# Kernel optimization log

Measured on AMD Instinct MI355X. Metric: run time of the kernel, lower is better.

Reference implementation:

```python
import jax, jax.numpy as jnp
import numpy as np

NUM_CLASSES = 1000
TEMPERATURE = 0.1
B, B_OOD, D = 4096, 4096, 512


def _l2norm(x):
    return x / jnp.linalg.norm(x, axis=-1, keepdims=True)


def setup_inputs() -> dict:
    key = jax.random.key(0)
    k1, k2, k3, k4, k5 = jax.random.split(key, 5)
    return {
        "centers1": _l2norm(jax.random.normal(k1, (NUM_CLASSES, D), dtype=jnp.float32)),
        "features": _l2norm(jax.random.normal(k2, (B, D), dtype=jnp.float32)),
        "targets": jax.random.randint(k3, (B,), 0, NUM_CLASSES, dtype=jnp.int64 if jax.config.jax_enable_x64 else jnp.int32),
        "features_ood": _l2norm(jax.random.normal(k4, (B_OOD, D), dtype=jnp.float32)),
        "pseudo_target_ood": jax.random.randint(k5, (B_OOD,), 0, NUM_CLASSES, dtype=jnp.int64 if jax.config.jax_enable_x64 else jnp.int32),
    }


def reference(centers1, features, targets, features_ood, pseudo_target_ood):
    C = centers1.shape[0]
    b = features.shape[0]
    bo = features_ood.shape[0]
    n = b + C + bo  # total anchors: batch + class centers + ood

    centers_lbl = jnp.arange(C, dtype=targets.dtype)
    ood_lbl = jnp.full((bo,), C, dtype=targets.dtype)  # ood gets label == num_classes
    targets_all = jnp.concatenate([targets, centers_lbl, ood_lbl])              # [N]
    targets_all_class = jnp.concatenate([targets, centers_lbl, pseudo_target_ood])  # [N]

    # per-class count over all N labels (pseudo labels for ood)
    batch_cls_count = jnp.zeros((C,), dtype=jnp.float32).at[targets_all_class].add(1.0)

    # positive mask: same label as anchor, excluding self (diagonal for j < B)
    mask = (targets_all[:b, None] == targets_all[None, :]).astype(jnp.float32)  # [B,N]
    logits_mask = 1.0 - (jnp.arange(n)[None, :] == jnp.arange(b)[:, None]).astype(jnp.float32)
    mask = mask * logits_mask

    features_all = jnp.concatenate([features, centers1, features_ood], axis=0)  # [N,D]
    logits = jnp.matmul(features, features_all.T) / TEMPERATURE                 # [B,N]
    logits = logits - jax.lax.stop_gradient(jnp.max(logits, axis=1, keepdims=True))

    exp_logits = jnp.exp(logits) * logits_mask
    # class-balanced per-instance weight (count of the column's class, minus positive mask)
    per_ins_weight = batch_cls_count[targets_all_class][None, :] - mask         # [B,N]
    exp_logits_sum = jnp.sum(exp_logits / per_ins_weight, axis=1, keepdims=True)
    log_prob = logits - jnp.log(exp_logits_sum)

    mean_log_prob_pos = jnp.sum(mask * log_prob, axis=1) / jnp.sum(mask, axis=1)
    loss = -jnp.mean(mean_log_prob_pos)
    return loss
```

## Files before the change

kernel.cpp:

```cpp
#include <hip/hip_runtime.h>
#include <stdint.h>

#define NUM_C 1000
#define NB    4096
#define NCOL  9192
#define NPAD  9216
#define DK    512
#define BM    128
#define BN    256
#define INV_T 10.0f

typedef __attribute__((ext_vector_type(4))) float f32x4;

#define OFF_FALL  0u
#define OFF_CNT   4718592u
#define OFF_CNTT  4722688u
#define OFF_S     4726784u
#define OFF_P     4743168u

__device__ __forceinline__ void async16(const void* g, void* l) {
  __builtin_amdgcn_global_load_lds((const __attribute__((address_space(1))) void*)g,
                                   (__attribute__((address_space(3))) void*)l,
                                   16, 0, 0);
}

__device__ __forceinline__ unsigned sw_e4m3(float x) {
  float ax = fabsf(x);
  unsigned s = (__float_as_uint(x) >> 24) & 0x80u;
  if (ax < 0.015625f) {
    int n = (int)rintf(ax * 512.0f);
    if (n >= 8) return s | 0x08u;
    return s | (unsigned)n;
  }
  if (ax >= 448.0f) return s | 0x7Eu;
  unsigned u = __float_as_uint(ax);
  int ee = (int)(u >> 23) - 127;
  float scale = __uint_as_float((unsigned)(3 - ee + 127) << 23);
  int qv = (int)rintf(ax * scale);
  if (qv == 16) { ee++; qv = 8; }
  return s | (unsigned)(((ee + 7) << 3) | (qv - 8));
}

template <bool HI>
__device__ __forceinline__ int cvt2(float a, float b, int old) {
#if __has_builtin(__builtin_amdgcn_cvt_pk_fp8_f32)
  return __builtin_amdgcn_cvt_pk_fp8_f32(a, b, old, HI);
#else
  unsigned pk = sw_e4m3(a) | (sw_e4m3(b) << 8);
  return HI ? (int)(((unsigned)old & 0x0000FFFFu) | (pk << 16))
            : (int)(((unsigned)old & 0xFFFF0000u) | pk);
#endif
}

__device__ __forceinline__ long long mk_ll(unsigned lo, unsigned hi) {
  return (long long)(((unsigned long long)hi << 32) | lo);
}

__global__ __launch_bounds__(256) void prep_k(const float* __restrict__ centers,
                                              const float* __restrict__ feats,
                                              const float* __restrict__ ood,
                                              const int* __restrict__ targets,
                                              const int* __restrict__ pseudo,
                                              uint4* __restrict__ fall,
                                              unsigned* __restrict__ cnt,
                                              unsigned* __restrict__ cntT,
                                              float* __restrict__ SP) {
  __shared__ unsigned hc[1024];
  __shared__ unsigned hct[1024];
  const int tid = threadIdx.x;

  int idx  = blockIdx.x * 256 + tid;
  int lane = idx & 63;
  int kp   = (idx >> 6) & 7;
  int t    = idx >> 9;
  int row  = t * 16 + (lane & 15);
  int k0   = kp * 64 + (lane >> 4) * 8;

  const float* src = nullptr;
  if (row < NB)              src = feats   + (size_t)row * DK;
  else if (row < NB + NUM_C) src = centers + (size_t)(row - NB) * DK;
  else if (row < NCOL)       src = ood     + (size_t)(row - NB - NUM_C) * DK;
  uint4 out = make_uint4(0u, 0u, 0u, 0u);
  if (src) {
    float4 v0 = *(const float4*)(src + k0);
    float4 v1 = *(const float4*)(src + k0 + 4);
    float4 v2 = *(const float4*)(src + k0 + 32);
    float4 v3 = *(const float4*)(src + k0 + 36);
    int p;
    p = 0; p = cvt2<false>(v0.x, v0.y, p); p = cvt2<true>(v0.z, v0.w, p); out.x = (unsigned)p;
    p = 0; p = cvt2<false>(v1.x, v1.y, p); p = cvt2<true>(v1.z, v1.w, p); out.y = (unsigned)p;
    p = 0; p = cvt2<false>(v2.x, v2.y, p); p = cvt2<true>(v2.z, v2.w, p); out.z = (unsigned)p;
    p = 0; p = cvt2<false>(v3.x, v3.y, p); p = cvt2<true>(v3.z, v3.w, p); out.w = (unsigned)p;
  }
  fall[idx] = out;

  if (blockIdx.x < 16) {
    for (int kk = tid; kk < 1024; kk += 256) { hc[kk] = 0u; hct[kk] = 0u; }
    __syncthreads();
    int i = blockIdx.x * 256 + tid;
    int tt = targets[i];
    atomicAdd(&hc[tt], 1u);
    atomicAdd(&hct[tt], 1u);
    atomicAdd(&hc[pseudo[i]], 1u);
    __syncthreads();
    for (int kk = tid; kk < 1024; kk += 256) {
      unsigned c = hc[kk], ct = hct[kk];
      if (c)  atomicAdd(&cnt[kk], c);
      if (ct) atomicAdd(&cntT[kk], ct);
    }
  } else if (blockIdx.x < 48) {
    SP[(blockIdx.x - 16) * 256 + tid] = 0.0f;
  }
}

__global__ __launch_bounds__(256, 2) void gemm_fused(const unsigned char* __restrict__ fall,
                                                     const int* __restrict__ targets,
                                                     const int* __restrict__ pseudo,
                                                     const unsigned* __restrict__ cnt,
                                                     float* __restrict__ Sacc,
                                                     float* __restrict__ Pacc) {
  __shared__ unsigned char Alds[65536];
  __shared__ int    sLbl[BN];
  __shared__ float  sRw0[BN];
  __shared__ float  sRw1[BN];
  __shared__ int    sTgt[BM];

  const int tid   = threadIdx.x;
  const int nTile = blockIdx.x;
  const int mTile = blockIdx.y;
  const int lane  = tid & 63;
  const int wv    = tid >> 6;
  const int wm    = wv >> 1;
  const int wn    = wv & 1;
  const int q     = lane >> 4;
  const int cIdx  = lane & 15;

  {
    const unsigned char* aSrc = fall + (size_t)(mTile * 8) * 8192;
#pragma unroll
    for (int i = 0; i < 16; i++)
      async16(aSrc + (i * 256 + tid) * 16, &Alds[(i * 256 + tid) * 16]);
  }

  {
    int j = nTile * BN + tid;
    int lbl, tac;
    if (j >= NCOL)         { lbl = -1; tac = -1; }
    else if (j < NB)       { tac = targets[j]; lbl = tac; }
    else if (j < NB+NUM_C) { tac = j - NB;     lbl = tac; }
    else                   { tac = pseudo[j - NB - NUM_C]; lbl = NUM_C; }
    sLbl[tid] = lbl;
    if (tac >= 0) {
      float w = (float)(1u + cnt[tac]);
      sRw0[tid] = 1.0f / w;
      sRw1[tid] = 1.0f / (w - 1.0f);
    } else {
      sRw0[tid] = 0.f;
      sRw1[tid] = 0.f;
    }
    if (tid < BM) sTgt[tid] = targets[mTile * BM + tid];
  }

  f32x4 acc[4][8];
#pragma unroll
  for (int mi = 0; mi < 4; mi++)
#pragma unroll
    for (int ni = 0; ni < 8; ni++)
      acc[mi][ni] = (f32x4){0.f, 0.f, 0.f, 0.f};

  const unsigned char* bBase = fall + (size_t)(nTile * 16 + wn * 8) * 8192 + lane * 16;
  const unsigned aBase = (unsigned)(wm * 4) * 8192u + (unsigned)lane * 16u;

  uint4 bCur[8], bNxt[8];
#pragma unroll
  for (int ni = 0; ni < 8; ni++)
    bCur[ni] = *(const uint4*)(bBase + ni * 8192);

  __syncthreads();

#pragma unroll
  for (int kp = 0; kp < 8; kp++) {
    if (kp < 7) {
#pragma unroll
      for (int ni = 0; ni < 8; ni++)
        bNxt[ni] = *(const uint4*)(bBase + ni * 8192 + (kp + 1) * 1024);
    }
    long long af0[4], af1[4];
#pragma unroll
    for (int mi = 0; mi < 4; mi++) {
      af0[mi] = *(const long long*)&Alds[aBase + mi * 8192 + kp * 1024];
      af1[mi] = *(const long long*)&Alds[aBase + mi * 8192 + kp * 1024 + 8];
    }
#pragma unroll
    for (int mi = 0; mi < 4; mi++)
#pragma unroll
      for (int ni = 0; ni < 8; ni++)
        acc[mi][ni] = __builtin_amdgcn_mfma_f32_16x16x32_fp8_fp8(af0[mi], mk_ll(bCur[ni].x, bCur[ni].y), acc[mi][ni], 0, 0, 0);
#pragma unroll
    for (int mi = 0; mi < 4; mi++)
#pragma unroll
      for (int ni = 0; ni < 8; ni++)
        acc[mi][ni] = __builtin_amdgcn_mfma_f32_16x16x32_fp8_fp8(af1[mi], mk_ll(bCur[ni].z, bCur[ni].w), acc[mi][ni], 0, 0, 0);
    if (kp < 7) {
#pragma unroll
      for (int ni = 0; ni < 8; ni++) bCur[ni] = bNxt[ni];
    }
  }

  float vS[16], vP[16];
#pragma unroll
  for (int s = 0; s < 16; s++) { vS[s] = 0.f; vP[s] = 0.f; }

#pragma unroll
  for (int ni = 0; ni < 8; ni++) {
    int jloc = wn * 128 + ni * 16 + cIdx;
    int j    = nTile * BN + jloc;
    int lblj = sLbl[jloc];
    float rw0 = sRw0[jloc], rw1 = sRw1[jloc];
#pragma unroll
    for (int mi = 0; mi < 4; mi++) {
      f32x4 a = acc[mi][ni];
#pragma unroll
      for (int r = 0; r < 4; r++) {
        int iloc = wm * 64 + mi * 16 + q * 4 + r;
        int i    = mTile * BM + iloc;
        int ti   = sTgt[iloc];
        float l  = a[r] * INV_T;
        bool diag = (j == i);
        bool pos  = (lblj == ti) && !diag;
        float rw  = diag ? 0.0f : (pos ? rw1 : rw0);
        float e   = __expf(l - 10.0f) * rw;
        vS[mi * 4 + r] += e;
        vP[mi * 4 + r] += pos ? l : 0.0f;
      }
    }
  }

#define RED_STEP(m, s, h)                                        \
  {                                                              \
    float sendS = (cIdx & (m)) ? vS[(s)] : vS[(s) + (h)];        \
    float sendP = (cIdx & (m)) ? vP[(s)] : vP[(s) + (h)];        \
    float rS = __shfl_xor(sendS, (m), 64);                       \
    float rP = __shfl_xor(sendP, (m), 64);                       \
    vS[(s)] = ((cIdx & (m)) ? vS[(s) + (h)] : vS[(s)]) + rS;     \
    vP[(s)] = ((cIdx & (m)) ? vP[(s) + (h)] : vP[(s)]) + rP;     \
  }
  RED_STEP(8, 0, 8) RED_STEP(8, 1, 8) RED_STEP(8, 2, 8) RED_STEP(8, 3, 8)
  RED_STEP(8, 4, 8) RED_STEP(8, 5, 8) RED_STEP(8, 6, 8) RED_STEP(8, 7, 8)
  RED_STEP(4, 0, 4) RED_STEP(4, 1, 4) RED_STEP(4, 2, 4) RED_STEP(4, 3, 4)
  RED_STEP(2, 0, 2) RED_STEP(2, 1, 2)
  RED_STEP(1, 0, 1)
#undef RED_STEP

  {
    int rowLoc = wm * 64 + (cIdx >> 2) * 16 + q * 4 + (cIdx & 3);
    int i = mTile * BM + rowLoc;
    atomicAdd(&Sacc[i], vS[0]);
    atomicAdd(&Pacc[i], vP[0]);
  }
}

__global__ __launch_bounds__(256) void finalize_k(const float* __restrict__ S,
                                                  const float* __restrict__ P,
                                                  const int* __restrict__ targets,
                                                  const unsigned* __restrict__ cntT,
                                                  float* __restrict__ out) {
  __shared__ unsigned ct[1024];
  __shared__ float red[4];
  int tid = threadIdx.x;
  for (int k = tid; k < 1024; k += 256) ct[k] = cntT[k];
  __syncthreads();
  float local = 0.f;
  for (int i = tid; i < NB; i += 256) {
    float npos = (float)ct[targets[i]];
    local += P[i] / npos - INV_T - __logf(S[i]);
  }
  for (int m = 1; m < 64; m <<= 1) local += __shfl_xor(local, m, 64);
  if ((tid & 63) == 0) red[tid >> 6] = local;
  __syncthreads();
  if (tid == 0) {
    float t = red[0] + red[1] + red[2] + red[3];
    out[0] = -t / (float)NB;
  }
}

extern "C" void kernel_launch(void* const* d_in, const int* in_sizes, int n_in,
                              void* d_out, int out_size, void* d_ws, size_t ws_size,
                              hipStream_t stream) {
  const float* centers = (const float*)d_in[0];
  const float* feats   = (const float*)d_in[1];
  const int*   targets = (const int*)d_in[2];
  const float* ood     = (const float*)d_in[3];
  const int*   pseudo  = (const int*)d_in[4];

  char* ws = (char*)d_ws;
  uint4*    fall  = (uint4*)(ws + OFF_FALL);
  unsigned* cnt   = (unsigned*)(ws + OFF_CNT);
  unsigned* cntT  = (unsigned*)(ws + OFF_CNTT);
  float*    Sacc  = (float*)(ws + OFF_S);
  float*    Pacc  = (float*)(ws + OFF_P);

  hipMemsetAsync(ws + OFF_CNT, 0, 8192, stream);
  prep_k<<<dim3((NPAD * 32) / 256), 256, 0, stream>>>(centers, feats, ood, targets, pseudo,
                                                      fall, cnt, cntT, Sacc);
  gemm_fused<<<dim3(NPAD / BN, NB / BM), 256, 0, stream>>>((const unsigned char*)fall, targets,
                                                           pseudo, cnt, Sacc, Pacc);
  finalize_k<<<1, 256, 0, stream>>>(Sacc, Pacc, targets, cntT, (float*)d_out);
}
```

Baseline: 120.9 us.

## Switch GEMM to 32x32x64 scaled FP8 MFMA with swizzled operand layout

Replaces the 16x16x32 FP8 MFMA with the MI355 32x32x64 f8f6f4 scaled MFMA using neutral scales. The prep kernel now writes operands in a new XOR-swizzled 32-row packed layout that matches this instruction, so LDS reads avoid bank conflicts. Workgroup indices are also remapped for better L2 reuse. The epilogue and row reduction are rewritten around the new 32x32 accumulator layout. The aim is fewer, denser matrix instructions and less LDS traffic, at the cost of a more intricate index mapping that must stay correct.

Measured after the change: 119.5 us. No clear change (-1.1%).

```diff
diff --git a/kernel.cpp b/kernel.cpp
--- a/kernel.cpp
+++ b/kernel.cpp
@@ -10,7 +10,8 @@
 #define BN    256
 #define INV_T 10.0f
 
-typedef __attribute__((ext_vector_type(4))) float f32x4;
+typedef __attribute__((ext_vector_type(16))) float f32x16;
+typedef __attribute__((ext_vector_type(8)))  int   i32x8;
 
 #define OFF_FALL  0u
 #define OFF_CNT   4718592u
@@ -52,9 +53,15 @@
 #endif
 }
 
-__device__ __forceinline__ long long mk_ll(unsigned lo, unsigned hi) {
-  return (long long)(((unsigned long long)hi << 32) | lo);
-}
+__device__ __forceinline__ i32x8 mk8(uint4 lo, uint4 hi) {
+  i32x8 r;
+  r[0] = (int)lo.x; r[1] = (int)lo.y; r[2] = (int)lo.z; r[3] = (int)lo.w;
+  r[4] = (int)hi.x; r[5] = (int)hi.y; r[6] = (int)hi.z; r[7] = (int)hi.w;
+  return r;
+}
+
+#define MFMA_SC(a, b, c) \
+  __builtin_amdgcn_mfma_scale_f32_32x32x64_f8f6f4((a), (b), (c), 0, 0, 0, 0x7F7F7F7F, 0, 0x7F7F7F7F)
 
 __global__ __launch_bounds__(256) void prep_k(const float* __restrict__ centers,
                                               const float* __restrict__ feats,
@@ -70,11 +77,13 @@
   const int tid = threadIdx.x;
 
   int idx  = blockIdx.x * 256 + tid;
-  int lane = idx & 63;
-  int kp   = (idx >> 6) & 7;
-  int t    = idx >> 9;
-  int row  = t * 16 + (lane & 15);
-  int k0   = kp * 64 + (lane >> 4) * 8;
+  int tile = idx >> 10;
+  int kq   = (idx >> 7) & 7;
+  int p    = idx & 127;
+  int c    = p ^ ((p >> 3) & 7);
+  int lane = c >> 1;
+  int row  = tile * 32 + (lane & 31);
+  int k0   = kq * 64 + (lane >> 5) * 32 + (c & 1) * 16;
 
   const float* src = nullptr;
   if (row < NB)              src = feats   + (size_t)row * DK;
@@ -84,13 +93,13 @@
   if (src) {
     float4 v0 = *(const float4*)(src + k0);
     float4 v1 = *(const float4*)(src + k0 + 4);
-    float4 v2 = *(const float4*)(src + k0 + 32);
-    float4 v3 = *(const float4*)(src + k0 + 36);
-    int p;
-    p = 0; p = cvt2<false>(v0.x, v0.y, p); p = cvt2<true>(v0.z, v0.w, p); out.x = (unsigned)p;
-    p = 0; p = cvt2<false>(v1.x, v1.y, p); p = cvt2<true>(v1.z, v1.w, p); out.y = (unsigned)p;
-    p = 0; p = cvt2<false>(v2.x, v2.y, p); p = cvt2<true>(v2.z, v2.w, p); out.z = (unsigned)p;
-    p = 0; p = cvt2<false>(v3.x, v3.y, p); p = cvt2<true>(v3.z, v3.w, p); out.w = (unsigned)p;
+    float4 v2 = *(const float4*)(src + k0 + 8);
+    float4 v3 = *(const float4*)(src + k0 + 12);
+    int q;
+    q = 0; q = cvt2<false>(v0.x, v0.y, q); q = cvt2<true>(v0.z, v0.w, q); out.x = (unsigned)q;
+    q = 0; q = cvt2<false>(v1.x, v1.y, q); q = cvt2<true>(v1.z, v1.w, q); out.y = (unsigned)q;
+    q = 0; q = cvt2<false>(v2.x, v2.y, q); q = cvt2<true>(v2.z, v2.w, q); out.z = (unsigned)q;
+    q = 0; q = cvt2<false>(v3.x, v3.y, q); q = cvt2<true>(v3.z, v3.w, q); out.w = (unsigned)q;
   }
   fall[idx] = out;
 
@@ -104,8 +113,8 @@
     atomicAdd(&hc[pseudo[i]], 1u);
     __syncthreads();
     for (int kk = tid; kk < 1024; kk += 256) {
-      unsigned c = hc[kk], ct = hct[kk];
-      if (c)  atomicAdd(&cnt[kk], c);
+      unsigned cc = hc[kk], ct = hct[kk];
+      if (cc) atomicAdd(&cnt[kk], cc);
       if (ct) atomicAdd(&cntT[kk], ct);
     }
   } else if (blockIdx.x < 48) {
@@ -125,18 +134,16 @@
   __shared__ float  sRw1[BN];
   __shared__ int    sTgt[BM];
 
-  const int tid   = threadIdx.x;
-  const int nTile = blockIdx.x;
-  const int mTile = blockIdx.y;
+  const int tid  = threadIdx.x;
+  int flat = (int)blockIdx.y * 36 + (int)blockIdx.x;
+  int swz  = (flat & 7) * 144 + (flat >> 3);
+  const int nTile = swz >> 5;
+  const int mTile = swz & 31;
   const int lane  = tid & 63;
   const int wv    = tid >> 6;
-  const int wm    = wv >> 1;
-  const int wn    = wv & 1;
-  const int q     = lane >> 4;
-  const int cIdx  = lane & 15;
 
   {
-    const unsigned char* aSrc = fall + (size_t)(mTile * 8) * 8192;
+    const unsigned char* aSrc = fall + (size_t)mTile * 65536;
 #pragma unroll
     for (int i = 0; i < 16; i++)
       async16(aSrc + (i * 256 + tid) * 16, &Alds[(i * 256 + tid) * 16]);
@@ -161,103 +168,107 @@
     if (tid < BM) sTgt[tid] = targets[mTile * BM + tid];
   }
 
-  f32x4 acc[4][8];
-#pragma unroll
-  for (int mi = 0; mi < 4; mi++)
-#pragma unroll
-    for (int ni = 0; ni < 8; ni++)
-      acc[mi][ni] = (f32x4){0.f, 0.f, 0.f, 0.f};
-
-  const unsigned char* bBase = fall + (size_t)(nTile * 16 + wn * 8) * 8192 + lane * 16;
-  const unsigned aBase = (unsigned)(wm * 4) * 8192u + (unsigned)lane * 16u;
-
-  uint4 bCur[8], bNxt[8];
-#pragma unroll
-  for (int ni = 0; ni < 8; ni++)
-    bCur[ni] = *(const uint4*)(bBase + ni * 8192);
+  f32x16 acc[4][2];
+  {
+    f32x16 z;
+#pragma unroll
+    for (int t = 0; t < 16; t++) z[t] = 0.f;
+#pragma unroll
+    for (int mi = 0; mi < 4; mi++) { acc[mi][0] = z; acc[mi][1] = z; }
+  }
+
+  const int swzo = ((lane >> 2) & 7) << 4;
+  const int off0 = (lane << 5) ^ swzo;
+  const int off1 = off0 ^ 16;
+
+  const unsigned char* bBase0 = fall + (size_t)(nTile * 8 + wv * 2) * 16384;
+  const unsigned char* bBase1 = bBase0 + 16384;
+
+  uint4 b0l = *(const uint4*)(bBase0 + off0);
+  uint4 b0h = *(const uint4*)(bBase0 + off1);
+  uint4 b1l = *(const uint4*)(bBase1 + off0);
+  uint4 b1h = *(const uint4*)(bBase1 + off1);
 
   __syncthreads();
 
 #pragma unroll
-  for (int kp = 0; kp < 8; kp++) {
-    if (kp < 7) {
-#pragma unroll
-      for (int ni = 0; ni < 8; ni++)
-        bNxt[ni] = *(const uint4*)(bBase + ni * 8192 + (kp + 1) * 1024);
-    }
-    long long af0[4], af1[4];
+  for (int kq = 0; kq < 8; kq++) {
+    uint4 n0l, n0h, n1l, n1h;
+    if (kq < 7) {
+      const unsigned char* pb0 = bBase0 + (kq + 1) * 2048;
+      const unsigned char* pb1 = bBase1 + (kq + 1) * 2048;
+      n0l = *(const uint4*)(pb0 + off0); n0h = *(const uint4*)(pb0 + off1);
+      n1l = *(const uint4*)(pb1 + off0); n1h = *(const uint4*)(pb1 + off1);
+    }
+    i32x8 bf0 = mk8(b0l, b0h);
+    i32x8 bf1 = mk8(b1l, b1h);
 #pragma unroll
     for (int mi = 0; mi < 4; mi++) {
-      af0[mi] = *(const long long*)&Alds[aBase + mi * 8192 + kp * 1024];
-      af1[mi] = *(const long long*)&Alds[aBase + mi * 8192 + kp * 1024 + 8];
-    }
-#pragma unroll
-    for (int mi = 0; mi < 4; mi++)
-#pragma unroll
-      for (int ni = 0; ni < 8; ni++)
-        acc[mi][ni] = __builtin_amdgcn_mfma_f32_16x16x32_fp8_fp8(af0[mi], mk_ll(bCur[ni].x, bCur[ni].y), acc[mi][ni], 0, 0, 0);
-#pragma unroll
-    for (int mi = 0; mi < 4; mi++)
-#pragma unroll
-      for (int ni = 0; ni < 8; ni++)
-        acc[mi][ni] = __builtin_amdgcn_mfma_f32_16x16x32_fp8_fp8(af1[mi], mk_ll(bCur[ni].z, bCur[ni].w), acc[mi][ni], 0, 0, 0);
-    if (kp < 7) {
-#pragma unroll
-      for (int ni = 0; ni < 8; ni++) bCur[ni] = bNxt[ni];
-    }
-  }
-
-  float vS[16], vP[16];
-#pragma unroll
-  for (int s = 0; s < 16; s++) { vS[s] = 0.f; vP[s] = 0.f; }
-
-#pragma unroll
-  for (int ni = 0; ni < 8; ni++) {
-    int jloc = wn * 128 + ni * 16 + cIdx;
-    int j    = nTile * BN + jloc;
-    int lblj = sLbl[jloc];
-    float rw0 = sRw0[jloc], rw1 = sRw1[jloc];
-#pragma unroll
-    for (int mi = 0; mi < 4; mi++) {
-      f32x4 a = acc[mi][ni];
-#pragma unroll
-      for (int r = 0; r < 4; r++) {
-        int iloc = wm * 64 + mi * 16 + q * 4 + r;
-        int i    = mTile * BM + iloc;
-        int ti   = sTgt[iloc];
-        float l  = a[r] * INV_T;
-        bool diag = (j == i);
-        bool pos  = (lblj == ti) && !diag;
-        float rw  = diag ? 0.0f : (pos ? rw1 : rw0);
-        float e   = __expf(l - 10.0f) * rw;
-        vS[mi * 4 + r] += e;
-        vP[mi * 4 + r] += pos ? l : 0.0f;
-      }
-    }
-  }
-
-#define RED_STEP(m, s, h)                                        \
-  {                                                              \
-    float sendS = (cIdx & (m)) ? vS[(s)] : vS[(s) + (h)];        \
-    float sendP = (cIdx & (m)) ? vP[(s)] : vP[(s) + (h)];        \
-    float rS = __shfl_xor(sendS, (m), 64);                       \
-    float rP = __shfl_xor(sendP, (m), 64);                       \
-    vS[(s)] = ((cIdx & (m)) ? vS[(s) + (h)] : vS[(s)]) + rS;     \
-    vP[(s)] = ((cIdx & (m)) ? vP[(s) + (h)] : vP[(s)]) + rP;     \
-  }
-  RED_STEP(8, 0, 8) RED_STEP(8, 1, 8) RED_STEP(8, 2, 8) RED_STEP(8, 3, 8)
-  RED_STEP(8, 4, 8) RED_STEP(8, 5, 8) RED_STEP(8, 6, 8) RED_STEP(8, 7, 8)
-  RED_STEP(4, 0, 4) RED_STEP(4, 1, 4) RED_STEP(4, 2, 4) RED_STEP(4, 3, 4)
-  RED_STEP(2, 0, 2) RED_STEP(2, 1, 2)
-  RED_STEP(1, 0, 1)
-#undef RED_STEP
-
-  {
-    int rowLoc = wm * 64 + (cIdx >> 2) * 16 + q * 4 + (cIdx & 3);
-    int i = mTile * BM + rowLoc;
-    atomicAdd(&Sacc[i], vS[0]);
-    atomicAdd(&Pacc[i], vP[0]);
-  }
+      const unsigned ao = (unsigned)mi * 16384u + (unsigned)kq * 2048u;
+      uint4 al = *(const uint4*)&Alds[ao + off0];
+      uint4 ah = *(const uint4*)&Alds[ao + off1];
+      i32x8 af = mk8(al, ah);
+      acc[mi][0] = MFMA_SC(af, bf0, acc[mi][0]);
+      acc[mi][1] = MFMA_SC(af, bf1, acc[mi][1]);
+    }
+    if (kq < 7) { b0l = n0l; b0h = n0h; b1l = n1l; b1h = n1h; }
+  }
+
+  const int cq = lane & 31;
+  const int hh = lane >> 5;
+  const int jl0 = wv * 64 + cq;
+  const int jl1 = jl0 + 32;
+  const int jg0 = nTile * BN + jl0;
+  const int jg1 = jg0 + 32;
+  const int lbl0 = sLbl[jl0], lbl1 = sLbl[jl1];
+  const float w00 = sRw0[jl0], w01 = sRw1[jl0];
+  const float w10 = sRw0[jl1], w11 = sRw1[jl1];
+
+#define RED(m, s, h)                                           \
+  {                                                            \
+    float sS = (lane & (m)) ? vS[(s)] : vS[(s) + (h)];         \
+    float sP = (lane & (m)) ? vP[(s)] : vP[(s) + (h)];         \
+    float rS = __shfl_xor(sS, (m), 64);                        \
+    float rP = __shfl_xor(sP, (m), 64);                        \
+    vS[(s)] = ((lane & (m)) ? vS[(s) + (h)] : vS[(s)]) + rS;   \
+    vP[(s)] = ((lane & (m)) ? vP[(s) + (h)] : vP[(s)]) + rP;   \
+  }
+
+#pragma unroll
+  for (int mi = 0; mi < 4; mi++) {
+    float vS[16], vP[16];
+#pragma unroll
+    for (int r = 0; r < 16; r++) {
+      int rowT = (r & 3) + 8 * (r >> 2) + 4 * hh;
+      int iloc = mi * 32 + rowT;
+      int ig   = mTile * BM + iloc;
+      int ti   = sTgt[iloc];
+      float l0 = acc[mi][0][r] * INV_T;
+      float l1 = acc[mi][1][r] * INV_T;
+      bool d0 = (jg0 == ig), d1 = (jg1 == ig);
+      bool p0 = (lbl0 == ti) && !d0;
+      bool p1 = (lbl1 == ti) && !d1;
+      float r0 = d0 ? 0.f : (p0 ? w01 : w00);
+      float r1 = d1 ? 0.f : (p1 ? w11 : w10);
+      vS[r] = __expf(l0 - 10.0f) * r0 + __expf(l1 - 10.0f) * r1;
+      vP[r] = (p0 ? l0 : 0.f) + (p1 ? l1 : 0.f);
+    }
+    RED(1, 0, 8) RED(1, 1, 8) RED(1, 2, 8) RED(1, 3, 8)
+    RED(1, 4, 8) RED(1, 5, 8) RED(1, 6, 8) RED(1, 7, 8)
+    RED(2, 0, 4) RED(2, 1, 4) RED(2, 2, 4) RED(2, 3, 4)
+    RED(4, 0, 2) RED(4, 1, 2)
+    RED(8, 0, 1)
+    vS[0] += __shfl_xor(vS[0], 16, 64);
+    vP[0] += __shfl_xor(vP[0], 16, 64);
+    if (!(lane & 16)) {
+      int rr   = ((lane & 1) << 3) | ((lane & 2) << 1) | ((lane & 4) >> 1) | ((lane & 8) >> 3);
+      int rowT = (rr & 3) + 8 * (rr >> 2) + 4 * hh;
+      int ig   = mTile * BM + mi * 32 + rowT;
+      atomicAdd(&Sacc[ig], vS[0]);
+      atomicAdd(&Pacc[ig], vP[0]);
+    }
+  }
+#undef RED
 }
 
 __global__ __launch_bounds__(256) void finalize_k(const float* __restrict__ S,
```
